# Kernel tuning notes

Measured on AMD Instinct MI355X. Metric: run time of the kernel, lower is better.

## Reference

```python
import jax, jax.numpy as jnp
import numpy as np

B, T = 32, 128
NQ, NC, DK, DA = 1000, 64, 128, 128


def _xavier(k, shape):
    bound = float(np.sqrt(6.0 / (shape[0] + shape[1])))
    return jax.random.uniform(k, shape, jnp.float32, -bound, bound)


def setup_inputs() -> dict:
    key = jax.random.key(0)
    ks = jax.random.split(key, 12)
    q_data = jax.random.randint(ks[0], (B, T), 0, NQ)
    a_data = (jax.random.uniform(ks[1], (B, T)) < 0.5).astype(jnp.float32)
    q_matrix = (jax.random.uniform(ks[2], (NQ + 10, NC)) < 0.1).astype(jnp.float32)
    q_embed_w = _xavier(ks[3], (NQ + 10, DK))
    W1 = _xavier(ks[4], (DK, DA + DK)); b1 = jnp.zeros((DK,), jnp.float32)
    W2 = _xavier(ks[5], (DK, 3 * DK)); b2 = jnp.zeros((DK,), jnp.float32)
    W3 = _xavier(ks[6], (DK, 3 * DK)); b3 = jnp.zeros((DK,), jnp.float32)
    W4 = _xavier(ks[7], (DK, 2 * DK)); b4 = jnp.zeros((DK,), jnp.float32)
    W5 = _xavier(ks[8], (DK, 2 * DK)); b5 = jnp.zeros((DK,), jnp.float32)
    h0 = _xavier(ks[9], (NC, DK))  # xavier init of the per-concept memory, shared across batch
    return dict(q_data=q_data, a_data=a_data, q_matrix=q_matrix, q_embed_w=q_embed_w,
                W1=W1, b1=b1, W2=W2, b2=b2, W3=W3, b3=b3, W4=W4, b4=b4, W5=W5, b5=b5, h0=h0)


def reference(q_data, a_data, q_matrix, q_embed_w, W1, b1, W2, b2, W3, b3, W4, b4, W5, b5, h0):
    Bn, Tn = q_data.shape
    dk = W1.shape[0]
    q_emb = q_embed_w[q_data]                                    # [B,T,dk]
    a_rep = jnp.broadcast_to(a_data[:, :, None], (Bn, Tn, DA))   # a repeated along d_a
    qa = jnp.concatenate([q_emb, a_rep], -1) @ W1.T + b1         # [B,T,dk]
    qm = q_matrix[q_data]                                        # [B,T,n_c]
    h_pre0 = jnp.broadcast_to(h0, (Bn,) + h0.shape)              # [B,n_c,dk]
    h_tilde0 = jnp.einsum('bn,bnd->bd', qm[:, 0], h_pre0)        # t=0 lazy init of h_tilde_pre
    learning0 = jnp.zeros((Bn, dk), q_emb.dtype)

    def step(carry, xs):
        learning_pre, h_pre, h_tilde_pre = carry
        q_e, q_e_next, learning, qemb_next = xs
        cat3 = jnp.concatenate([learning_pre, learning, h_tilde_pre], -1)  # [B,3dk]
        KP = jnp.tanh(cat3 @ W2.T + b2)
        R = jax.nn.sigmoid(cat3 @ W3.T + b3)
        KC = R * (KP + 1.0) * 0.5                                # [B,dk]
        KC_tilde = q_e[:, :, None] * KC[:, None, :]              # outer-product memory write [B,n_c,dk]
        KC_b = jnp.broadcast_to(KC[:, None, :], h_pre.shape)
        KR = jax.nn.sigmoid(jnp.concatenate([h_pre, KC_b], -1) @ W4.T + b4) * h_pre
        h = KC_tilde + KR                                        # [B,n_c,dk]
        h_tilde = jnp.einsum('bn,bnd->bd', q_e_next, h)          # memory read for next item
        y = jax.nn.sigmoid(jnp.concatenate([qemb_next, h_tilde], -1) @ W5.T + b5).sum(-1) / dk
        return (learning, h, h_tilde), (h_pre, y)

    xs = (jnp.swapaxes(qm[:, :-1], 0, 1),    # q_e for t=0..T-2
          jnp.swapaxes(qm[:, 1:], 0, 1),     # q_e at t+1
          jnp.swapaxes(qa[:, :-1], 0, 1),    # learning_t
          jnp.swapaxes(q_emb[:, 1:], 0, 1))  # q_embed at t+1
    _, (H, ys) = jax.lax.scan(step, (learning0, h_pre0, h_tilde0), xs)
    H = jax.nn.sigmoid(H)                                        # [T-1,B,n_c,dk], matches torch stacking
    pred = jnp.concatenate([jnp.zeros((Bn, 1), ys.dtype), ys.T], axis=1)  # pred[:,0]=0
    return (H, pred, q_emb, qa)
```

## Files before the change

kernel.cpp:

```cpp
#include <hip/hip_runtime.h>

#define B_  32
#define T_  128
#define HFS 132
#define HBS 136

typedef __attribute__((ext_vector_type(8))) short bf16x8;
typedef __attribute__((ext_vector_type(4))) float f32x4;

__device__ __forceinline__ float sigf(float x){ return __builtin_amdgcn_rcpf(1.f + __expf(-x)); }
__device__ __forceinline__ float tanh_f(float x){ return 2.f*__builtin_amdgcn_rcpf(1.f + __expf(-2.f*x)) - 1.f; }
__device__ __forceinline__ unsigned short f2b(float x){
  union { float f; unsigned int u; } v; v.f = x;
  return (unsigned short)((v.u + 0x7FFFu + ((v.u >> 16) & 1u)) >> 16);
}
__device__ __forceinline__ float b2f(unsigned short u){
  union { unsigned int x; float f; } v; v.x = ((unsigned int)u) << 16; return v.f;
}
__device__ __forceinline__ void bar_lds(){
  __builtin_amdgcn_sched_barrier(0);
  asm volatile("s_waitcnt lgkmcnt(0)" ::: "memory");
  __builtin_amdgcn_s_barrier();
  __builtin_amdgcn_sched_barrier(0);
}

__global__ __launch_bounds__(256) void stage_k(
    const float* __restrict__ W2, const float* __restrict__ W3,
    const float* __restrict__ W4, const float* __restrict__ W1,
    unsigned short* __restrict__ W2b, unsigned short* __restrict__ W3b,
    unsigned short* __restrict__ W4b, float* __restrict__ S)
{
  int i = blockIdx.x*256 + threadIdx.x;
  if (i < 128*384){ W2b[i] = f2b(W2[i]); W3b[i] = f2b(W3[i]); }
  if (i < 128*256){ W4b[i] = f2b(W4[i]); }
  if (i < 128){
    float s = 0.f;
    const float* row = W1 + (size_t)i*256 + 128;
    for (int k = 0; k < 128; ++k) s += row[k];
    S[i] = s;
  }
}

__global__ __launch_bounds__(256) void prep_k(
    const int* __restrict__ qd, const float* __restrict__ ad,
    const float* __restrict__ qew, const float* __restrict__ W1,
    const float* __restrict__ b1, const float* __restrict__ S,
    float* __restrict__ oqe, float* __restrict__ oqa, float* __restrict__ pred)
{
  __shared__ float qe[16][128];
  __shared__ float w1c[128][65];
  const int tid = threadIdx.x;
  const int bt0 = blockIdx.x * 16;

  for (int i = tid; i < 16*128; i += 256){
    int r = i >> 7, d = i & 127;
    float v = qew[(size_t)qd[bt0 + r]*128 + d];
    qe[r][d] = v;
    oqe[(size_t)(bt0 + r)*128 + d] = v;
  }
  const int j = tid & 127, rh = tid >> 7;
  float accv[8];
  {
    float base = b1[j], Sj = S[j];
#pragma unroll
    for (int r = 0; r < 8; ++r) accv[r] = fmaf(ad[bt0 + rh*8 + r], Sj, base);
  }
  for (int c = 0; c < 2; ++c){
    __syncthreads();
    for (int i = tid; i < 128*64; i += 256){
      int jj = i >> 6, kk = i & 63;
      w1c[jj][kk] = W1[(size_t)jj*256 + c*64 + kk];
    }
    __syncthreads();
#pragma unroll 4
    for (int k = 0; k < 64; ++k){
      float wv = w1c[j][k];
#pragma unroll
      for (int r = 0; r < 8; ++r) accv[r] = fmaf(qe[rh*8 + r][c*64 + k], wv, accv[r]);
    }
  }
#pragma unroll
  for (int r = 0; r < 8; ++r) oqa[(size_t)(bt0 + rh*8 + r)*128 + j] = accv[r];
  if (blockIdx.x == 0 && tid < 32) pred[tid * T_] = 0.f;
}

__global__ __launch_bounds__(512) void l23_k(
    const float* __restrict__ oqa,
    const unsigned short* __restrict__ W2b, const unsigned short* __restrict__ W3b,
    const float* __restrict__ b2, const float* __restrict__ b3,
    unsigned short* __restrict__ L2b, unsigned short* __restrict__ L3b)
{
  __shared__ unsigned short qab[129*136];
  const int b = blockIdx.x, tid = threadIdx.x;
  const int w = tid >> 6, lane = tid & 63, g = lane >> 4, li = lane & 15;
  const int mw = w & 3, nw = w >> 2;

  for (int i = tid; i < 129*128; i += 512){
    int row = i >> 7, k = i & 127;
    qab[row*136 + k] = row ? f2b(oqa[((size_t)b*T_ + row-1)*128 + k]) : (unsigned short)0;
  }
  __syncthreads();

  const unsigned short* Wp[2] = {W2b, W3b};
  const float*          bp[2] = {b2, b3};
  unsigned short*       Lp[2] = {L2b, L3b};
#pragma unroll
  for (int m_ = 0; m_ < 2; ++m_){
    bf16x8 bfr[4][8];
#pragma unroll
    for (int nt4 = 0; nt4 < 4; ++nt4){
      int j = (nw*4 + nt4)*16 + li;
#pragma unroll
      for (int ks = 0; ks < 8; ++ks)
        bfr[nt4][ks] = *(const bf16x8*)(Wp[m_] + (size_t)j*384 + ks*32 + 8*g);
    }
    f32x4 acc[2][4] = {{{0,0,0,0},{0,0,0,0},{0,0,0,0},{0,0,0,0}},
                       {{0,0,0,0},{0,0,0,0},{0,0,0,0},{0,0,0,0}}};
#pragma unroll
    for (int mt2 = 0; mt2 < 2; ++mt2){
      int row = (mw*2 + mt2)*16 + li;
      bf16x8 afr[8];
#pragma unroll
      for (int ks = 0; ks < 4; ++ks){
        afr[ks]   = *(const bf16x8*)&qab[ row   *136 + ks*32 + 8*g];
        afr[ks+4] = *(const bf16x8*)&qab[(row+1)*136 + ks*32 + 8*g];
      }
#pragma unroll
      for (int ks = 0; ks < 8; ++ks)
#pragma unroll
        for (int nt4 = 0; nt4 < 4; ++nt4)
          acc[mt2][nt4] = __builtin_amdgcn_mfma_f32_16x16x32_bf16(afr[ks], bfr[nt4][ks], acc[mt2][nt4], 0,0,0);
    }
    float bias[4];
#pragma unroll
    for (int nt4 = 0; nt4 < 4; ++nt4) bias[nt4] = bp[m_][(nw*4 + nt4)*16 + li];
#pragma unroll
    for (int mt2 = 0; mt2 < 2; ++mt2)
#pragma unroll
      for (int nt4 = 0; nt4 < 4; ++nt4)
#pragma unroll
        for (int r = 0; r < 4; ++r){
          int t = (mw*2 + mt2)*16 + g*4 + r;
          int j = (nw*4 + nt4)*16 + li;
          if (t < 127) Lp[m_][((size_t)b*127 + t)*128 + j] = f2b(acc[mt2][nt4][r] + bias[nt4]);
        }
  }
}

struct __align__(16) SmR {
  float hfs[64*HFS];
  unsigned short hb[2][64*HBS];
  float qe[3][64];
  unsigned short htb[128];
  unsigned short kcb[128];
  int qdl[T_];
};

__global__ __launch_bounds__(512) void recur_k(
    const int* __restrict__ qd, const float* __restrict__ qmx,
    const float* __restrict__ h0, const float* __restrict__ b4,
    const unsigned short* __restrict__ W2b, const unsigned short* __restrict__ W3b,
    const unsigned short* __restrict__ W4b,
    const unsigned short* __restrict__ L2b, const unsigned short* __restrict__ L3b,
    float* __restrict__ H, unsigned short* __restrict__ HTg)
{
  __shared__ SmR s;
  const int b   = blockIdx.x;
  const int tid = threadIdx.x;
  const int w = tid >> 6, lane = tid & 63, g = lane >> 4, li = lane & 15;
  const int j = w*16 + li;

  bf16x8 w2cf[4], w3cf[4];
#pragma unroll
  for (int ks = 0; ks < 4; ++ks){
    w2cf[ks] = *(const bf16x8*)(W2b + (size_t)j*384 + 256 + ks*32 + 8*g);
    w3cf[ks] = *(const bf16x8*)(W3b + (size_t)j*384 + 256 + ks*32 + 8*g);
  }
  bf16x8 w4f[8];
#pragma unroll
  for (int ks = 0; ks < 8; ++ks)
    w4f[ks] = *(const bf16x8*)(W4b + (size_t)j*256 + ks*32 + 8*g);
  const float b4v = b4[j];

  float hreg[4][4];
#pragma unroll
  for (int mt = 0; mt < 4; ++mt)
#pragma unroll
    for (int r = 0; r < 4; ++r)
      hreg[mt][r] = h0[(mt*16 + g*4 + r)*128 + j];

  for (int i = tid; i < 64*128; i += 512){
    int n = i >> 7, d = i & 127;
    float v = h0[i];
    s.hb[0][n*HBS + d] = f2b(v);
    H[(size_t)b*8192 + i] = sigf(v);
  }
  if (tid < T_) s.qdl[tid] = qd[b*T_ + tid];
  __syncthreads();
  if (tid < 64){
    s.qe[0][tid] = qmx[(size_t)s.qdl[0]*64 + tid];
    s.qe[1][tid] = qmx[(size_t)s.qdl[1]*64 + tid];
  }
  __syncthreads();
  if (tid < 128){
    float acc = 0.f;
    for (int n = 0; n < 64; ++n) acc = fmaf(s.qe[0][n], h0[n*128 + tid], acc);
    s.htb[tid] = f2b(acc);
  }
  __syncthreads();

  float l2v = b2f(L2b[((size_t)b*127)*128 + j]);
  float l3v = b2f(L3b[((size_t)b*127)*128 + j]);

#pragma unroll 1
  for (int t = 0; t < T_-1; ++t){
    const int cur = t & 1, nxt = cur ^ 1;

    int tp1 = (t+1 < 127) ? t+1 : 126;
    unsigned short l2n = L2b[((size_t)b*127 + tp1)*128 + j];
    unsigned short l3n = L3b[((size_t)b*127 + tp1)*128 + j];
    float qmxv = 0.f;
    if (tid < 64 && t+2 < T_) qmxv = qmx[(size_t)s.qdl[t+2]*64 + tid];

    bf16x8 av[4];
#pragma unroll
    for (int ks = 0; ks < 4; ++ks) av[ks] = *(const bf16x8*)&s.htb[ks*32 + 8*g];
    f32x4 a2a = {0,0,0,0}, a2b = {0,0,0,0}, a3a = {0,0,0,0}, a3b = {0,0,0,0};
    a2a = __builtin_amdgcn_mfma_f32_16x16x32_bf16(av[0], w2cf[0], a2a, 0,0,0);
    a3a = __builtin_amdgcn_mfma_f32_16x16x32_bf16(av[0], w3cf[0], a3a, 0,0,0);
    a2b = __builtin_amdgcn_mfma_f32_16x16x32_bf16(av[1], w2cf[1], a2b, 0,0,0);
    a3b = __builtin_amdgcn_mfma_f32_16x16x32_bf16(av[1], w3cf[1], a3b, 0,0,0);
    a2a = __builtin_amdgcn_mfma_f32_16x16x32_bf16(av[2], w2cf[2], a2a, 0,0,0);
    a3a = __builtin_amdgcn_mfma_f32_16x16x32_bf16(av[2], w3cf[2], a3a, 0,0,0);
    a2b = __builtin_amdgcn_mfma_f32_16x16x32_bf16(av[3], w2cf[3], a2b, 0,0,0);
    a3b = __builtin_amdgcn_mfma_f32_16x16x32_bf16(av[3], w3cf[3], a3b, 0,0,0);
    float kp = tanh_f(a2a[0] + a2b[0] + l2v);
    float rr = sigf (a3a[0] + a3b[0] + l3v);
    float kc = rr*(kp + 1.f)*0.5f;
    if (g == 0) s.kcb[j] = f2b(kc);

    bf16x8 af[4][4];
#pragma unroll
    for (int mt = 0; mt < 4; ++mt)
#pragma unroll
      for (int ks = 0; ks < 4; ++ks)
        af[mt][ks] = *(const bf16x8*)&s.hb[cur][(mt*16 + li)*HBS + ks*32 + 8*g];
    f32x4 acc[4] = {{0,0,0,0},{0,0,0,0},{0,0,0,0},{0,0,0,0}};
#pragma unroll
    for (int ks = 0; ks < 4; ++ks)
#pragma unroll
      for (int mt = 0; mt < 4; ++mt)
        acc[mt] = __builtin_amdgcn_mfma_f32_16x16x32_bf16(af[mt][ks], w4f[ks], acc[mt], 0,0,0);

    if (t >= 1){
      float* Ho = H + ((size_t)t*B_ + b)*8192;
#pragma unroll
      for (int k = 0; k < 4; ++k){
        int f = tid + k*512;
        int n = f >> 5, d = (f & 31)*4;
        f32x4 v = *(const f32x4*)&s.hfs[n*HFS + d];
        v[0] = sigf(v[0]); v[1] = sigf(v[1]); v[2] = sigf(v[2]); v[3] = sigf(v[3]);
        *(f32x4*)&Ho[n*128 + d] = v;
      }
    }
    f32x4 qc4[4], qn4[4];
#pragma unroll
    for (int mt = 0; mt < 4; ++mt){
      qc4[mt] = *(const f32x4*)&s.qe[t%3][mt*16 + g*4];
      qn4[mt] = *(const f32x4*)&s.qe[(t+1)%3][mt*16 + g*4];
    }
    bar_lds();

    bf16x8 kf[4];
#pragma unroll
    for (int ks = 0; ks < 4; ++ks) kf[ks] = *(const bf16x8*)&s.kcb[ks*32 + 8*g];
    f32x4 acck = {0,0,0,0};
#pragma unroll
    for (int ks = 0; ks < 4; ++ks)
      acck = __builtin_amdgcn_mfma_f32_16x16x32_bf16(kf[ks], w4f[ks+4], acck, 0,0,0);

    float part = 0.f;
#pragma unroll
    for (int mt = 0; mt < 4; ++mt){
#pragma unroll
      for (int r = 0; r < 4; ++r){
        int n = mt*16 + g*4 + r;
        float sg = sigf(acc[mt][r] + acck[0] + b4v);
        float hn = fmaf(qc4[mt][r], kc, sg*hreg[mt][r]);
        hreg[mt][r] = hn;
        s.hfs[n*HFS + j]     = hn;
        s.hb[nxt][n*HBS + j] = f2b(hn);
        part = fmaf(qn4[mt][r], hn, part);
      }
    }
    part += __shfl_xor(part, 16);
    part += __shfl_xor(part, 32);
    if (g == 0){
      unsigned short hb16 = f2b(part);
      s.htb[j] = hb16;
      HTg[((size_t)b*T_ + t + 1)*128 + j] = hb16;
    }
    if (tid < 64 && t+2 < T_) s.qe[(t+2)%3][tid] = qmxv;
    l2v = b2f(l2n); l3v = b2f(l3n);
    bar_lds();
  }
}

__global__ __launch_bounds__(256) void ypost_k(
    const float* __restrict__ oqe, const unsigned short* __restrict__ HT,
    const float* __restrict__ W5, const float* __restrict__ b5,
    float* __restrict__ pred)
{
  __shared__ float X[32][256];
  __shared__ float w5c[128][33];
  const int tau = blockIdx.x + 1;
  const int tid = threadIdx.x;

  for (int i = tid; i < 32*128; i += 256){
    int bb = i >> 7, k = i & 127;
    X[bb][k] = oqe[((size_t)bb*T_ + tau)*128 + k];
    X[bb][128 + k] = b2f(HT[((size_t)bb*T_ + tau)*128 + k]);
  }
  const int j = tid & 127, rh = tid >> 7;
  float acc[16];
  float base = b5[j];
#pragma unroll
  for (int r = 0; r < 16; ++r) acc[r] = base;
  for (int c = 0; c < 8; ++c){
    __syncthreads();
    for (int i = tid; i < 128*32; i += 256){
      int jj = i >> 5, kk = i & 31;
      w5c[jj][kk] = W5[(size_t)jj*256 + c*32 + kk];
    }
    __syncthreads();
#pragma unroll 8
    for (int k = 0; k < 32; ++k){
      float wv = w5c[j][k];
#pragma unroll
      for (int r = 0; r < 16; ++r) acc[r] = fmaf(X[rh*16 + r][c*32 + k], wv, acc[r]);
    }
  }
  __syncthreads();
#pragma unroll
  for (int r = 0; r < 16; ++r) X[rh*16 + r][j] = sigf(acc[r]);
  __syncthreads();
  if (tid < 32){
    float ssum = 0.f;
    for (int k = 0; k < 128; ++k) ssum += X[tid][k];
    pred[tid*T_ + tau] = ssum * (1.f/128.f);
  }
}

extern "C" void kernel_launch(void* const* d_in, const int* in_sizes, int n_in,
                              void* d_out, int out_size, void* d_ws, size_t ws_size,
                              hipStream_t stream)
{
  const int*   qd  = (const int*)  d_in[0];
  const float* ad  = (const float*)d_in[1];
  const float* qmx = (const float*)d_in[2];
  const float* qew = (const float*)d_in[3];
  const float* W1  = (const float*)d_in[4];
  const float* b1  = (const float*)d_in[5];
  const float* W2  = (const float*)d_in[6];
  const float* b2  = (const float*)d_in[7];
  const float* W3  = (const float*)d_in[8];
  const float* b3  = (const float*)d_in[9];
  const float* W4  = (const float*)d_in[10];
  const float* b4  = (const float*)d_in[11];
  const float* W5  = (const float*)d_in[12];
  const float* b5  = (const float*)d_in[13];
  const float* h0  = (const float*)d_in[14];

  float* H    = (float*)d_out;
  float* pred = H    + (size_t)127*32*64*128;
  float* oqe  = pred + (size_t)32*128;
  float* oqa  = oqe  + (size_t)32*128*128;

  unsigned short* W2b = (unsigned short*)d_ws;
  unsigned short* W3b = W2b + 128*384;
  unsigned short* W4b = W3b + 128*384;
  unsigned short* HTg = W4b + 128*256;
  unsigned short* L2b = HTg + (size_t)32*128*128;
  unsigned short* L3b = L2b + (size_t)32*127*128;
  float*          S   = (float*)(L3b + (size_t)32*127*128);

  stage_k<<<192, 256, 0, stream>>>(W2, W3, W4, W1, W2b, W3b, W4b, S);
  prep_k <<<256, 256, 0, stream>>>(qd, ad, qew, W1, b1, S, oqe, oqa, pred);
  l23_k  <<<32,  512, 0, stream>>>(oqa, W2b, W3b, b2, b3, L2b, L3b);
  recur_k<<<32,  512, 0, stream>>>(qd, qmx, h0, b4, W2b, W3b, W4b, L2b, L3b, H, HTg);
  ypost_k<<<127, 256, 0, stream>>>(oqe, HTg, W5, b5, pred);
}
```

Baseline: 408.2 us.

## Fuse output prediction into recurrence kernel and drop fp32 H shadow buffer

Removes the separate ypost kernel and computes each step's W5 projection, sigmoid and sum inside the recurrent loop, using MFMA against W5 fragments held in registers. This drops the HTg global round-trip and one launch. The H output is now written from the bf16 LDS copy instead of an fp32 shadow buffer, which saves LDS and writes but lowers H precision to bf16 rounding. MFMA chains are also split into independent accumulators to shorten dependency latency, at the cost of more registers in the serial loop.

Result: faster. 395.3 us (-3.2%).

```diff
diff --git a/kernel.cpp b/kernel.cpp
--- a/kernel.cpp
+++ b/kernel.cpp
@@ -2,11 +2,11 @@
 
 #define B_  32
 #define T_  128
-#define HFS 132
 #define HBS 136
 
 typedef __attribute__((ext_vector_type(8))) short bf16x8;
 typedef __attribute__((ext_vector_type(4))) float f32x4;
+typedef __attribute__((ext_vector_type(4))) unsigned short u16x4;
 
 __device__ __forceinline__ float sigf(float x){ return __builtin_amdgcn_rcpf(1.f + __expf(-x)); }
 __device__ __forceinline__ float tanh_f(float x){ return 2.f*__builtin_amdgcn_rcpf(1.f + __expf(-2.f*x)) - 1.f; }
@@ -26,13 +26,15 @@
 
 __global__ __launch_bounds__(256) void stage_k(
     const float* __restrict__ W2, const float* __restrict__ W3,
-    const float* __restrict__ W4, const float* __restrict__ W1,
+    const float* __restrict__ W4, const float* __restrict__ W5,
+    const float* __restrict__ W1,
     unsigned short* __restrict__ W2b, unsigned short* __restrict__ W3b,
-    unsigned short* __restrict__ W4b, float* __restrict__ S)
+    unsigned short* __restrict__ W4b, unsigned short* __restrict__ W5b,
+    float* __restrict__ S)
 {
   int i = blockIdx.x*256 + threadIdx.x;
   if (i < 128*384){ W2b[i] = f2b(W2[i]); W3b[i] = f2b(W3[i]); }
-  if (i < 128*256){ W4b[i] = f2b(W4[i]); }
+  if (i < 128*256){ W4b[i] = f2b(W4[i]); W5b[i] = f2b(W5[i]); }
   if (i < 128){
     float s = 0.f;
     const float* row = W1 + (size_t)i*256 + 128;
@@ -148,21 +150,24 @@
 }
 
 struct __align__(16) SmR {
-  float hfs[64*HFS];
   unsigned short hb[2][64*HBS];
   float qe[3][64];
+  float yp[8];
   unsigned short htb[128];
   unsigned short kcb[128];
+  unsigned short ybq[128];
   int qdl[T_];
 };
 
 __global__ __launch_bounds__(512) void recur_k(
     const int* __restrict__ qd, const float* __restrict__ qmx,
     const float* __restrict__ h0, const float* __restrict__ b4,
+    const float* __restrict__ b5,
     const unsigned short* __restrict__ W2b, const unsigned short* __restrict__ W3b,
-    const unsigned short* __restrict__ W4b,
+    const unsigned short* __restrict__ W4b, const unsigned short* __restrict__ W5b,
     const unsigned short* __restrict__ L2b, const unsigned short* __restrict__ L3b,
-    float* __restrict__ H, unsigned short* __restrict__ HTg)
+    const float* __restrict__ oqe,
+    float* __restrict__ H, float* __restrict__ pred)
 {
   __shared__ SmR s;
   const int b   = blockIdx.x;
@@ -180,7 +185,11 @@
 #pragma unroll
   for (int ks = 0; ks < 8; ++ks)
     w4f[ks] = *(const bf16x8*)(W4b + (size_t)j*256 + ks*32 + 8*g);
-  const float b4v = b4[j];
+  bf16x8 w5f[8];
+#pragma unroll
+  for (int ks = 0; ks < 8; ++ks)
+    w5f[ks] = *(const bf16x8*)(W5b + (size_t)j*256 + ks*32 + 8*g);
+  const float b4v = b4[j], b5v = b5[j];
 
   float hreg[4][4];
 #pragma unroll
@@ -196,6 +205,7 @@
     H[(size_t)b*8192 + i] = sigf(v);
   }
   if (tid < T_) s.qdl[tid] = qd[b*T_ + tid];
+  if (tid < 128) s.ybq[tid] = 0;
   __syncthreads();
   if (tid < 64){
     s.qe[0][tid] = qmx[(size_t)s.qdl[0]*64 + tid];
@@ -219,25 +229,44 @@
     int tp1 = (t+1 < 127) ? t+1 : 126;
     unsigned short l2n = L2b[((size_t)b*127 + tp1)*128 + j];
     unsigned short l3n = L3b[((size_t)b*127 + tp1)*128 + j];
-    float qmxv = 0.f;
+    float qmxv = 0.f, qen = 0.f;
     if (tid < 64 && t+2 < T_) qmxv = qmx[(size_t)s.qdl[t+2]*64 + tid];
+    if (tid < 128)            qen  = oqe[((size_t)b*T_ + t+1)*128 + tid];
 
     bf16x8 av[4];
 #pragma unroll
     for (int ks = 0; ks < 4; ++ks) av[ks] = *(const bf16x8*)&s.htb[ks*32 + 8*g];
-    f32x4 a2a = {0,0,0,0}, a2b = {0,0,0,0}, a3a = {0,0,0,0}, a3b = {0,0,0,0};
-    a2a = __builtin_amdgcn_mfma_f32_16x16x32_bf16(av[0], w2cf[0], a2a, 0,0,0);
-    a3a = __builtin_amdgcn_mfma_f32_16x16x32_bf16(av[0], w3cf[0], a3a, 0,0,0);
-    a2b = __builtin_amdgcn_mfma_f32_16x16x32_bf16(av[1], w2cf[1], a2b, 0,0,0);
-    a3b = __builtin_amdgcn_mfma_f32_16x16x32_bf16(av[1], w3cf[1], a3b, 0,0,0);
-    a2a = __builtin_amdgcn_mfma_f32_16x16x32_bf16(av[2], w2cf[2], a2a, 0,0,0);
-    a3a = __builtin_amdgcn_mfma_f32_16x16x32_bf16(av[2], w3cf[2], a3a, 0,0,0);
-    a2b = __builtin_amdgcn_mfma_f32_16x16x32_bf16(av[3], w2cf[3], a2b, 0,0,0);
-    a3b = __builtin_amdgcn_mfma_f32_16x16x32_bf16(av[3], w3cf[3], a3b, 0,0,0);
-    float kp = tanh_f(a2a[0] + a2b[0] + l2v);
-    float rr = sigf (a3a[0] + a3b[0] + l3v);
+
+    f32x4 q2[4], q3[4];
+#pragma unroll
+    for (int ks = 0; ks < 4; ++ks){
+      f32x4 z = {0,0,0,0};
+      q2[ks] = __builtin_amdgcn_mfma_f32_16x16x32_bf16(av[ks], w2cf[ks], z, 0,0,0);
+      q3[ks] = __builtin_amdgcn_mfma_f32_16x16x32_bf16(av[ks], w3cf[ks], z, 0,0,0);
+    }
+    float kp = tanh_f((q2[0][0]+q2[1][0]) + (q2[2][0]+q2[3][0]) + l2v);
+    float rr = sigf ((q3[0][0]+q3[1][0]) + (q3[2][0]+q3[3][0]) + l3v);
     float kc = rr*(kp + 1.f)*0.5f;
     if (g == 0) s.kcb[j] = f2b(kc);
+
+    {
+      bf16x8 yq[4];
+#pragma unroll
+      for (int ks = 0; ks < 4; ++ks) yq[ks] = *(const bf16x8*)&s.ybq[ks*32 + 8*g];
+      f32x4 y_[8];
+#pragma unroll
+      for (int ks = 0; ks < 4; ++ks){
+        f32x4 z = {0,0,0,0};
+        y_[ks]   = __builtin_amdgcn_mfma_f32_16x16x32_bf16(yq[ks], w5f[ks],   z, 0,0,0);
+        y_[ks+4] = __builtin_amdgcn_mfma_f32_16x16x32_bf16(av[ks], w5f[ks+4], z, 0,0,0);
+      }
+      float o5 = ((y_[0][0]+y_[1][0]) + (y_[2][0]+y_[3][0]))
+               + ((y_[4][0]+y_[5][0]) + (y_[6][0]+y_[7][0]));
+      float sv = sigf(o5 + b5v);
+      sv += __shfl_xor(sv, 1); sv += __shfl_xor(sv, 2);
+      sv += __shfl_xor(sv, 4); sv += __shfl_xor(sv, 8);
+      if (lane == 0) s.yp[w] = sv;
+    }
 
     bf16x8 af[4][4];
 #pragma unroll
@@ -256,11 +285,13 @@
       float* Ho = H + ((size_t)t*B_ + b)*8192;
 #pragma unroll
       for (int k = 0; k < 4; ++k){
-        int f = tid + k*512;
-        int n = f >> 5, d = (f & 31)*4;
-        f32x4 v = *(const f32x4*)&s.hfs[n*HFS + d];
-        v[0] = sigf(v[0]); v[1] = sigf(v[1]); v[2] = sigf(v[2]); v[3] = sigf(v[3]);
-        *(f32x4*)&Ho[n*128 + d] = v;
+        int c = tid + k*512;
+        int n = c >> 5, o = (c & 31)*4;
+        u16x4 hv = *(const u16x4*)&s.hb[cur][n*HBS + o];
+        f32x4 v;
+        v[0] = sigf(b2f(hv[0])); v[1] = sigf(b2f(hv[1]));
+        v[2] = sigf(b2f(hv[2])); v[3] = sigf(b2f(hv[3]));
+        *(f32x4*)&Ho[n*128 + o] = v;
       }
     }
     f32x4 qc4[4], qn4[4];
@@ -274,10 +305,13 @@
     bf16x8 kf[4];
 #pragma unroll
     for (int ks = 0; ks < 4; ++ks) kf[ks] = *(const bf16x8*)&s.kcb[ks*32 + 8*g];
-    f32x4 acck = {0,0,0,0};
-#pragma unroll
-    for (int ks = 0; ks < 4; ++ks)
-      acck = __builtin_amdgcn_mfma_f32_16x16x32_bf16(kf[ks], w4f[ks+4], acck, 0,0,0);
+    f32x4 zk[4];
+#pragma unroll
+    for (int ks = 0; ks < 4; ++ks){
+      f32x4 z = {0,0,0,0};
+      zk[ks] = __builtin_amdgcn_mfma_f32_16x16x32_bf16(kf[ks], w4f[ks+4], z, 0,0,0);
+    }
+    float ack = (zk[0][0]+zk[1][0]) + (zk[2][0]+zk[3][0]);
 
     float part = 0.f;
 #pragma unroll
@@ -285,69 +319,54 @@
 #pragma unroll
       for (int r = 0; r < 4; ++r){
         int n = mt*16 + g*4 + r;
-        float sg = sigf(acc[mt][r] + acck[0] + b4v);
+        float sg = sigf(acc[mt][r] + ack + b4v);
         float hn = fmaf(qc4[mt][r], kc, sg*hreg[mt][r]);
         hreg[mt][r] = hn;
-        s.hfs[n*HFS + j]     = hn;
         s.hb[nxt][n*HBS + j] = f2b(hn);
         part = fmaf(qn4[mt][r], hn, part);
       }
     }
     part += __shfl_xor(part, 16);
     part += __shfl_xor(part, 32);
-    if (g == 0){
-      unsigned short hb16 = f2b(part);
-      s.htb[j] = hb16;
-      HTg[((size_t)b*T_ + t + 1)*128 + j] = hb16;
-    }
+    if (g == 0) s.htb[j] = f2b(part);
+
+    if (w == 0 && lane < 8){
+      float v = s.yp[lane];
+      v += __shfl_xor(v, 4); v += __shfl_xor(v, 2); v += __shfl_xor(v, 1);
+      if (lane == 0 && t >= 1) pred[b*T_ + t] = v * (1.f/128.f);
+    }
+    if (tid < 128) s.ybq[tid] = f2b(qen);
     if (tid < 64 && t+2 < T_) s.qe[(t+2)%3][tid] = qmxv;
     l2v = b2f(l2n); l3v = b2f(l3n);
     bar_lds();
   }
-}
-
-__global__ __launch_bounds__(256) void ypost_k(
-    const float* __restrict__ oqe, const unsigned short* __restrict__ HT,
-    const float* __restrict__ W5, const float* __restrict__ b5,
-    float* __restrict__ pred)
-{
-  __shared__ float X[32][256];
-  __shared__ float w5c[128][33];
-  const int tau = blockIdx.x + 1;
-  const int tid = threadIdx.x;
-
-  for (int i = tid; i < 32*128; i += 256){
-    int bb = i >> 7, k = i & 127;
-    X[bb][k] = oqe[((size_t)bb*T_ + tau)*128 + k];
-    X[bb][128 + k] = b2f(HT[((size_t)bb*T_ + tau)*128 + k]);
-  }
-  const int j = tid & 127, rh = tid >> 7;
-  float acc[16];
-  float base = b5[j];
-#pragma unroll
-  for (int r = 0; r < 16; ++r) acc[r] = base;
-  for (int c = 0; c < 8; ++c){
-    __syncthreads();
-    for (int i = tid; i < 128*32; i += 256){
-      int jj = i >> 5, kk = i & 31;
-      w5c[jj][kk] = W5[(size_t)jj*256 + c*32 + kk];
-    }
-    __syncthreads();
-#pragma unroll 8
-    for (int k = 0; k < 32; ++k){
-      float wv = w5c[j][k];
-#pragma unroll
-      for (int r = 0; r < 16; ++r) acc[r] = fmaf(X[rh*16 + r][c*32 + k], wv, acc[r]);
-    }
-  }
-  __syncthreads();
-#pragma unroll
-  for (int r = 0; r < 16; ++r) X[rh*16 + r][j] = sigf(acc[r]);
-  __syncthreads();
-  if (tid < 32){
-    float ssum = 0.f;
-    for (int k = 0; k < 128; ++k) ssum += X[tid][k];
-    pred[tid*T_ + tau] = ssum * (1.f/128.f);
+
+  {
+    bf16x8 av[4], yq[4];
+#pragma unroll
+    for (int ks = 0; ks < 4; ++ks){
+      av[ks] = *(const bf16x8*)&s.htb[ks*32 + 8*g];
+      yq[ks] = *(const bf16x8*)&s.ybq[ks*32 + 8*g];
+    }
+    f32x4 y_[8];
+#pragma unroll
+    for (int ks = 0; ks < 4; ++ks){
+      f32x4 z = {0,0,0,0};
+      y_[ks]   = __builtin_amdgcn_mfma_f32_16x16x32_bf16(yq[ks], w5f[ks],   z, 0,0,0);
+      y_[ks+4] = __builtin_amdgcn_mfma_f32_16x16x32_bf16(av[ks], w5f[ks+4], z, 0,0,0);
+    }
+    float o5 = ((y_[0][0]+y_[1][0]) + (y_[2][0]+y_[3][0]))
+             + ((y_[4][0]+y_[5][0]) + (y_[6][0]+y_[7][0]));
+    float sv = sigf(o5 + b5v);
+    sv += __shfl_xor(sv, 1); sv += __shfl_xor(sv, 2);
+    sv += __shfl_xor(sv, 4); sv += __shfl_xor(sv, 8);
+    if (lane == 0) s.yp[w] = sv;
+  }
+  bar_lds();
+  if (w == 0 && lane < 8){
+    float v = s.yp[lane];
+    v += __shfl_xor(v, 4); v += __shfl_xor(v, 2); v += __shfl_xor(v, 1);
+    if (lane == 0) pred[b*T_ + 127] = v * (1.f/128.f);
   }
 }
 
@@ -379,14 +398,14 @@
   unsigned short* W2b = (unsigned short*)d_ws;
   unsigned short* W3b = W2b + 128*384;
   unsigned short* W4b = W3b + 128*384;
-  unsigned short* HTg = W4b + 128*256;
-  unsigned short* L2b = HTg + (size_t)32*128*128;
+  unsigned short* W5b = W4b + 128*256;
+  unsigned short* L2b = W5b + 128*256;
   unsigned short* L3b = L2b + (size_t)32*127*128;
   float*          S   = (float*)(L3b + (size_t)32*127*128);
 
-  stage_k<<<192, 256, 0, stream>>>(W2, W3, W4, W1, W2b, W3b, W4b, S);
+  stage_k<<<192, 256, 0, stream>>>(W2, W3, W4, W5, W1, W2b, W3b, W4b, W5b, S);
   prep_k <<<256, 256, 0, stream>>>(qd, ad, qew, W1, b1, S, oqe, oqa, pred);
   l23_k  <<<32,  512, 0, stream>>>(oqa, W2b, W3b, b2, b3, L2b, L3b);
-  recur_k<<<32,  512, 0, stream>>>(qd, qmx, h0, b4, W2b, W3b, W4b, L2b, L3b, H, HTg);
-  ypost_k<<<127, 256, 0, stream>>>(oqe, HTg, W5, b5, pred);
-}
+  recur_k<<<32,  512, 0, stream>>>(qd, qmx, h0, b4, b5, W2b, W3b, W4b, W5b,
+                                   L2b, L3b, oqe, H, pred);
+}
```

## Defer H sigmoid expansion to a separate parallel kernel, storing bf16 in recurrence

Applied to the files above, without the earlier changes.

The serial recurrence kernel no longer keeps an fp32 copy of the memory state in LDS or applies the sigmoid and fp32 store to H each step. Instead it writes the bf16 state into the first half of each H slot, and a new wide-grid kernel expands it to sigmoid fp32 in place. This moves half the bytes and all the transcendental work off the 32-block latency-bound loop. The MFMA chains are also split into independent accumulators to shorten the dependency chain, and the qe vector is carried in registers. H output now derives from bf16-rounded state, which adds precision loss, and an extra kernel launch.

New measurement: 371.1 us. 1.1x faster.

```diff
diff --git a/kernel.cpp b/kernel.cpp
--- a/kernel.cpp
+++ b/kernel.cpp
@@ -2,11 +2,11 @@
 
 #define B_  32
 #define T_  128
-#define HFS 132
 #define HBS 136
 
 typedef __attribute__((ext_vector_type(8))) short bf16x8;
 typedef __attribute__((ext_vector_type(4))) float f32x4;
+typedef __attribute__((ext_vector_type(8))) unsigned short u16x8;
 
 __device__ __forceinline__ float sigf(float x){ return __builtin_amdgcn_rcpf(1.f + __expf(-x)); }
 __device__ __forceinline__ float tanh_f(float x){ return 2.f*__builtin_amdgcn_rcpf(1.f + __expf(-2.f*x)) - 1.f; }
@@ -148,7 +148,6 @@
 }
 
 struct __align__(16) SmR {
-  float hfs[64*HFS];
   unsigned short hb[2][64*HBS];
   float qe[3][64];
   unsigned short htb[128];
@@ -211,6 +210,9 @@
 
   float l2v = b2f(L2b[((size_t)b*127)*128 + j]);
   float l3v = b2f(L3b[((size_t)b*127)*128 + j]);
+  f32x4 qc4[4];
+#pragma unroll
+  for (int mt = 0; mt < 4; ++mt) qc4[mt] = *(const f32x4*)&s.qe[0][mt*16 + g*4];
 
 #pragma unroll 1
   for (int t = 0; t < T_-1; ++t){
@@ -225,17 +227,15 @@
     bf16x8 av[4];
 #pragma unroll
     for (int ks = 0; ks < 4; ++ks) av[ks] = *(const bf16x8*)&s.htb[ks*32 + 8*g];
-    f32x4 a2a = {0,0,0,0}, a2b = {0,0,0,0}, a3a = {0,0,0,0}, a3b = {0,0,0,0};
-    a2a = __builtin_amdgcn_mfma_f32_16x16x32_bf16(av[0], w2cf[0], a2a, 0,0,0);
-    a3a = __builtin_amdgcn_mfma_f32_16x16x32_bf16(av[0], w3cf[0], a3a, 0,0,0);
-    a2b = __builtin_amdgcn_mfma_f32_16x16x32_bf16(av[1], w2cf[1], a2b, 0,0,0);
-    a3b = __builtin_amdgcn_mfma_f32_16x16x32_bf16(av[1], w3cf[1], a3b, 0,0,0);
-    a2a = __builtin_amdgcn_mfma_f32_16x16x32_bf16(av[2], w2cf[2], a2a, 0,0,0);
-    a3a = __builtin_amdgcn_mfma_f32_16x16x32_bf16(av[2], w3cf[2], a3a, 0,0,0);
-    a2b = __builtin_amdgcn_mfma_f32_16x16x32_bf16(av[3], w2cf[3], a2b, 0,0,0);
-    a3b = __builtin_amdgcn_mfma_f32_16x16x32_bf16(av[3], w3cf[3], a3b, 0,0,0);
-    float kp = tanh_f(a2a[0] + a2b[0] + l2v);
-    float rr = sigf (a3a[0] + a3b[0] + l3v);
+    f32x4 q2[4], q3[4];
+#pragma unroll
+    for (int ks = 0; ks < 4; ++ks){
+      f32x4 z = {0,0,0,0};
+      q2[ks] = __builtin_amdgcn_mfma_f32_16x16x32_bf16(av[ks], w2cf[ks], z, 0,0,0);
+      q3[ks] = __builtin_amdgcn_mfma_f32_16x16x32_bf16(av[ks], w3cf[ks], z, 0,0,0);
+    }
+    float kp = tanh_f((q2[0][0]+q2[1][0]) + (q2[2][0]+q2[3][0]) + l2v);
+    float rr = sigf ((q3[0][0]+q3[1][0]) + (q3[2][0]+q3[3][0]) + l3v);
     float kc = rr*(kp + 1.f)*0.5f;
     if (g == 0) s.kcb[j] = f2b(kc);
 
@@ -253,31 +253,31 @@
         acc[mt] = __builtin_amdgcn_mfma_f32_16x16x32_bf16(af[mt][ks], w4f[ks], acc[mt], 0,0,0);
 
     if (t >= 1){
-      float* Ho = H + ((size_t)t*B_ + b)*8192;
-#pragma unroll
-      for (int k = 0; k < 4; ++k){
-        int f = tid + k*512;
-        int n = f >> 5, d = (f & 31)*4;
-        f32x4 v = *(const f32x4*)&s.hfs[n*HFS + d];
-        v[0] = sigf(v[0]); v[1] = sigf(v[1]); v[2] = sigf(v[2]); v[3] = sigf(v[3]);
-        *(f32x4*)&Ho[n*128 + d] = v;
+      unsigned short* Hu = (unsigned short*)(H + ((size_t)t*B_ + b)*8192);
+#pragma unroll
+      for (int k = 0; k < 2; ++k){
+        int c = tid + k*512;
+        int n = c >> 4, o = (c & 15)*8;
+        u16x8 hv = *(const u16x8*)&s.hb[cur][n*HBS + o];
+        *(u16x8*)&Hu[c*8] = hv;
       }
     }
-    f32x4 qc4[4], qn4[4];
-#pragma unroll
-    for (int mt = 0; mt < 4; ++mt){
-      qc4[mt] = *(const f32x4*)&s.qe[t%3][mt*16 + g*4];
+    f32x4 qn4[4];
+#pragma unroll
+    for (int mt = 0; mt < 4; ++mt)
       qn4[mt] = *(const f32x4*)&s.qe[(t+1)%3][mt*16 + g*4];
-    }
     bar_lds();
 
     bf16x8 kf[4];
 #pragma unroll
     for (int ks = 0; ks < 4; ++ks) kf[ks] = *(const bf16x8*)&s.kcb[ks*32 + 8*g];
-    f32x4 acck = {0,0,0,0};
-#pragma unroll
-    for (int ks = 0; ks < 4; ++ks)
-      acck = __builtin_amdgcn_mfma_f32_16x16x32_bf16(kf[ks], w4f[ks+4], acck, 0,0,0);
+    f32x4 zk[4];
+#pragma unroll
+    for (int ks = 0; ks < 4; ++ks){
+      f32x4 z = {0,0,0,0};
+      zk[ks] = __builtin_amdgcn_mfma_f32_16x16x32_bf16(kf[ks], w4f[ks+4], z, 0,0,0);
+    }
+    float ack = (zk[0][0]+zk[1][0]) + (zk[2][0]+zk[3][0]);
 
     float part = 0.f;
 #pragma unroll
@@ -285,10 +285,9 @@
 #pragma unroll
       for (int r = 0; r < 4; ++r){
         int n = mt*16 + g*4 + r;
-        float sg = sigf(acc[mt][r] + acck[0] + b4v);
+        float sg = sigf(acc[mt][r] + ack + b4v);
         float hn = fmaf(qc4[mt][r], kc, sg*hreg[mt][r]);
         hreg[mt][r] = hn;
-        s.hfs[n*HFS + j]     = hn;
         s.hb[nxt][n*HBS + j] = f2b(hn);
         part = fmaf(qn4[mt][r], hn, part);
       }
@@ -302,7 +301,37 @@
     }
     if (tid < 64 && t+2 < T_) s.qe[(t+2)%3][tid] = qmxv;
     l2v = b2f(l2n); l3v = b2f(l3n);
+#pragma unroll
+    for (int mt = 0; mt < 4; ++mt) qc4[mt] = qn4[mt];
     bar_lds();
+  }
+}
+
+__global__ __launch_bounds__(256) void hexp_k(float* __restrict__ H)
+{
+  const int tb = blockIdx.x;
+  const int t  = (tb >> 5) + 1, b = tb & 31;
+  float* Hs = H + ((size_t)t*B_ + b)*8192;
+  const unsigned short* Hu = (const unsigned short*)Hs;
+  const int tid = threadIdx.x;
+
+  u16x8 v[4];
+#pragma unroll
+  for (int k = 0; k < 4; ++k){
+    int c = k*256 + tid;
+    v[k] = *(const u16x8*)&Hu[c*8];
+  }
+  __syncthreads();
+#pragma unroll
+  for (int k = 0; k < 4; ++k){
+    int c = k*256 + tid;
+    f32x4 lo, hi;
+    lo[0]=sigf(b2f(v[k][0])); lo[1]=sigf(b2f(v[k][1]));
+    lo[2]=sigf(b2f(v[k][2])); lo[3]=sigf(b2f(v[k][3]));
+    hi[0]=sigf(b2f(v[k][4])); hi[1]=sigf(b2f(v[k][5]));
+    hi[2]=sigf(b2f(v[k][6])); hi[3]=sigf(b2f(v[k][7]));
+    *(f32x4*)&Hs[c*8]     = lo;
+    *(f32x4*)&Hs[c*8 + 4] = hi;
   }
 }
 
@@ -387,6 +416,8 @@
   stage_k<<<192, 256, 0, stream>>>(W2, W3, W4, W1, W2b, W3b, W4b, S);
   prep_k <<<256, 256, 0, stream>>>(qd, ad, qew, W1, b1, S, oqe, oqa, pred);
   l23_k  <<<32,  512, 0, stream>>>(oqa, W2b, W3b, b2, b3, L2b, L3b);
-  recur_k<<<32,  512, 0, stream>>>(qd, qmx, h0, b4, W2b, W3b, W4b, L2b, L3b, H, HTg);
+  recur_k<<<32,  512, 0, stream>>>(qd, qmx, h0, b4, W2b, W3b, W4b,
+                                   L2b, L3b, H, HTg);
+  hexp_k <<<126*32, 256, 0, stream>>>(H);
   ypost_k<<<127, 256, 0, stream>>>(oqe, HTg, W5, b5, pred);
 }
```
